# Kernel optimization log

Measured on AMD Instinct MI355X. Metric: run time of the kernel, lower is better.

## Reference

```python
import jax, jax.numpy as jnp
import numpy as np

N = 50000      # num_nodes
E = 800000     # num_edges
D = 128        # hidden_dim
POOL_RATIO = 0.5
CROSS_W = 1.0  # cross_weight


def _gcn(x, W, b, src, dst, n):
    """GCNConv: symmetric-normalized aggregation with self-loops. Dropout is identity (eval)."""
    loops = jnp.arange(n)
    s = jnp.concatenate([src, loops])
    d = jnp.concatenate([dst, loops])
    deg = jax.ops.segment_sum(jnp.ones(s.shape, x.dtype), d, num_segments=n)
    inv_sqrt = jax.lax.rsqrt(jnp.maximum(deg, 1.0))  # deg >= 1 due to self-loops
    xw = x @ W                                        # [n, D]
    msg = xw[s] * (inv_sqrt[s] * inv_sqrt[d])[:, None]  # [E+n, D] gather
    return jax.ops.segment_sum(msg, d, num_segments=n) + b


def _prelu(x, a):
    return jnp.where(x >= 0, x, a * x)


def setup_inputs() -> dict:
    key = jax.random.key(0)
    ks = jax.random.split(key, 8)
    glorot = lambda k, sh: jax.random.normal(k, sh, jnp.float32) * np.float32(np.sqrt(2.0 / (sh[0] + sh[1])))
    return {
        "feat": jax.random.normal(ks[0], (N, D), jnp.float32),
        "h_neg": jax.random.normal(ks[1], (N, D), jnp.float32),
        "edge_index": jax.random.randint(ks[2], (2, E), 0, N),
        "Wd": glorot(ks[3], (D, D)),
        "bd": jnp.zeros((D,), jnp.float32),
        "prelu_a": jnp.full((1,), 0.25, jnp.float32),
        "Wbil": glorot(ks[4], (D, D)),
        "bbil": jnp.zeros((1,), jnp.float32),
        "Wg1": glorot(ks[5], (D, D)),
        "bg1": jnp.zeros((D,), jnp.float32),
        "Wg2": glorot(ks[6], (D, D)),
        "bg2": jnp.zeros((D,), jnp.float32),
        "Wg3": glorot(ks[7], (D, D)),
        "bg3": jnp.zeros((D,), jnp.float32),
    }


def reference(feat, h_neg, edge_index, Wd, bd, prelu_a, Wbil, bbil,
              Wg1, bg1, Wg2, bg2, Wg3, bg3):
    src, dst = edge_index[0], edge_index[1]
    # --- IndexSelect: dense layer on pos/neg features ---
    h_pos = _prelu(feat @ Wd + bd, prelu_a)
    h_neg_d = _prelu(h_neg @ Wd + bd, prelu_a)
    embed = _gcn(h_pos, Wg1, bg1, src, dst, N)
    h_center = jax.nn.sigmoid(embed)
    # Discriminator (bilinear) positive scores -> node importance
    score_pos = jnp.einsum('nd,de,ne->n', h_pos, Wbil, h_center) + bbil[0]
    _ = jnp.einsum('nd,de,ne->n', h_neg_d, Wbil, h_center) + bbil[0]  # score_neg (logits branch)
    scores = jax.nn.sigmoid(score_pos)
    order = jnp.argsort(-scores)           # descending
    k = int(POOL_RATIO * N)
    select_idx = order[:k]
    select_scores = scores[order][:k]
    # --- GraphPool (use_gcn=True): down-sample GCN, gather, scale ---
    pooled = _gcn(embed, Wg2, bg2, src, dst, N)[select_idx] * select_scores[:, None]
    # --- GraphUnpool: scatter into zeros, up-sample GCN ---
    fine = jnp.zeros((N, D), feat.dtype).at[select_idx].set(pooled)
    out = _gcn(fine, Wg3, bg3, src, dst, N)
    # --- cross/fuse connection ---
    return out + CROSS_W * embed
```

## Files before the change

### kernel.cpp

```cpp
#include <hip/hip_runtime.h>
#include <hip/hip_bf16.h>

#define NN 50000
#define NE 800000
#define DD 128
#define KSEL 25000
#define NBK 391
#define NBLKA 98

typedef unsigned int uint32;
typedef unsigned short ushort16;

__device__ __forceinline__ float sigmoidf(float x){ return 1.f/(1.f+__expf(-x)); }

__device__ __forceinline__ unsigned short f2b(float f){
  union{float f; unsigned u;} v; v.f=f;
  unsigned r=(v.u + 0x7fffu + ((v.u>>16)&1u))>>16;
  return (unsigned short)r;
}

__device__ __forceinline__ void addbf2(float&lo,float&hi,uint32 u,float w){
  lo+=__uint_as_float(u<<16)*w;
  hi+=__uint_as_float(u&0xffff0000u)*w;
}

__global__ __launch_bounds__(1024) void k_bcount(const int* __restrict__ dst,
    int* __restrict__ btot, int* __restrict__ blkcnt){
  __shared__ int h[NBK];
  int tid=threadIdx.x;
  for(int i=tid;i<NBK;i+=1024) h[i]=0;
  __syncthreads();
  int e0=blockIdx.x*8192;
  #pragma unroll
  for(int t=0;t<8;t++){
    int e=e0+t*1024+tid;
    if(e<NE) atomicAdd(&h[dst[e]>>7],1);
  }
  __syncthreads();
  for(int i=tid;i<NBK;i+=1024){
    int c=h[i];
    blkcnt[blockIdx.x*NBK+i]=c;
    if(c) atomicAdd(&btot[i],c);
  }
}

__global__ __launch_bounds__(512) void k_bscan(const int* __restrict__ btot,
    int* __restrict__ boff, const int* __restrict__ blkcnt, int* __restrict__ blkbase,
    int* __restrict__ row_start){
  __shared__ int sdata[512];
  int tid=threadIdx.x;
  int v=(tid<NBK)?btot[tid]:0;
  sdata[tid]=v; __syncthreads();
  for(int off=1;off<512;off<<=1){
    int y=(tid>=off)?sdata[tid-off]:0;
    __syncthreads();
    sdata[tid]+=y;
    __syncthreads();
  }
  int excl=sdata[tid]-v;
  if(tid<NBK) boff[tid]=excl;
  if(tid==NBK-1){ boff[NBK]=excl+v; row_start[NN]=NE; }
  if(tid<NBK){
    int run=excl;
    for(int b=0;b<NBLKA;b++){
      int c=blkcnt[b*NBK+tid];
      blkbase[b*NBK+tid]=run;
      run+=c;
    }
  }
}

__global__ __launch_bounds__(1024) void k_bscatter(const int* __restrict__ src,
    const int* __restrict__ dst, const int* __restrict__ blkbase, uint32* __restrict__ pairs){
  __shared__ int cur[NBK];
  int tid=threadIdx.x;
  for(int i=tid;i<NBK;i+=1024) cur[i]=blkbase[blockIdx.x*NBK+i];
  __syncthreads();
  int e0=blockIdx.x*8192;
  #pragma unroll
  for(int t=0;t<8;t++){
    int e=e0+t*1024+tid;
    if(e<NE){
      int d=dst[e];
      int p=atomicAdd(&cur[d>>7],1);
      pairs[p]=(unsigned)src[e] | ((unsigned)(d&127)<<17);
    }
  }
}

__global__ __launch_bounds__(256) void k_bfinal(const uint32* __restrict__ pairs,
    const int* __restrict__ boff, int* __restrict__ row_start,
    float* __restrict__ inv_sq, int* __restrict__ csr_src){
  __shared__ int degl[128];
  __shared__ int cur[128];
  __shared__ int ssum[2];
  int b=blockIdx.x, tid=threadIdx.x;
  int lo=boff[b], hi=boff[b+1];
  if(tid<128) degl[tid]=0;
  __syncthreads();
  for(int e=lo+tid;e<hi;e+=256) atomicAdd(&degl[pairs[e]>>17],1);
  __syncthreads();
  int v=0,x=0;
  if(tid<128){
    v=degl[tid]; x=v;
    #pragma unroll
    for(int off=1;off<64;off<<=1){
      int y=__shfl_up(x,off,64);
      if((tid&63)>=off) x+=y;
    }
    if((tid&63)==63) ssum[tid>>6]=x;
  }
  __syncthreads();
  if(tid<128){
    int incl=x+((tid>=64)?ssum[0]:0);
    int node=b*128+tid;
    int excl=lo+incl-v;
    if(node<NN){
      row_start[node]=excl;
      cur[tid]=excl;
      inv_sq[node]=1.f/sqrtf((float)(v+1));
    }
  }
  __syncthreads();
  for(int e=lo+tid;e<hi;e+=256){
    uint32 u=pairs[e];
    int p=atomicAdd(&cur[u>>17],1);
    csr_src[p]=(int)(u&0x1FFFFu);
  }
}

__global__ void k_transpose(const float* __restrict__ W, float* __restrict__ Wt){
  int idx=blockIdx.x*256+threadIdx.x;
  if(idx<DD*DD){
    int k=idx>>7, c=idx&127;
    Wt[idx]=W[c*DD+k];
  }
}

template<int IN_SIG,int ACT,int OUT_BF16,int FUSE_SCORE>
__global__ __launch_bounds__(256) void k_gemm128(const float* __restrict__ A,
    const float* __restrict__ W, const float* __restrict__ bias,
    float* __restrict__ outf, ushort16* __restrict__ outb,
    const float* __restrict__ aparam, const float* __restrict__ hp,
    const float* __restrict__ bbil, float* __restrict__ score){
  __shared__ float Al[128][132];
  int tid=threadIdx.x;
  int row0=blockIdx.x*128;
  {
    const float4* A4=(const float4*)(A+(size_t)row0*DD);
    #pragma unroll
    for(int i=0;i<16;i++){
      int idx=i*256+tid;
      int r=idx>>5, c=(idx&31)*4;
      float4 v=make_float4(0.f,0.f,0.f,0.f);
      if(row0+r<NN) v=A4[idx];
      if(IN_SIG){ v.x=sigmoidf(v.x); v.y=sigmoidf(v.y); v.z=sigmoidf(v.z); v.w=sigmoidf(v.w); }
      *(float4*)&Al[r][c]=v;
    }
  }
  __syncthreads();
  int tx=tid&15, ty=tid>>4;
  float acc[8][8];
  #pragma unroll
  for(int i=0;i<8;i++)
    #pragma unroll
    for(int c=0;c<8;c++) acc[i][c]=0.f;

  for(int k=0;k<DD;k+=4){
    float wv[4][8];
    #pragma unroll
    for(int r=0;r<4;r++){
      float4 lo=*(const float4*)&W[(size_t)(k+r)*DD+tx*8];
      float4 hi=*(const float4*)&W[(size_t)(k+r)*DD+tx*8+4];
      wv[r][0]=lo.x; wv[r][1]=lo.y; wv[r][2]=lo.z; wv[r][3]=lo.w;
      wv[r][4]=hi.x; wv[r][5]=hi.y; wv[r][6]=hi.z; wv[r][7]=hi.w;
    }
    #pragma unroll
    for(int i=0;i<8;i++){
      float4 a=*(const float4*)&Al[ty+16*i][k];
      #pragma unroll
      for(int c=0;c<8;c++)
        acc[i][c]+=a.x*wv[0][c]+a.y*wv[1][c]+a.z*wv[2][c]+a.w*wv[3][c];
    }
  }

  if(FUSE_SCORE){
    float bb=bbil[0];
    #pragma unroll
    for(int i=0;i<8;i++){
      int r=row0+ty+16*i;
      float p=0.f;
      if(r<NN){
        float4 h0=*(const float4*)&hp[(size_t)r*DD+tx*8];
        float4 h1=*(const float4*)&hp[(size_t)r*DD+tx*8+4];
        p=acc[i][0]*h0.x+acc[i][1]*h0.y+acc[i][2]*h0.z+acc[i][3]*h0.w
         +acc[i][4]*h1.x+acc[i][5]*h1.y+acc[i][6]*h1.z+acc[i][7]*h1.w;
      }
      p+=__shfl_xor(p,1,64); p+=__shfl_xor(p,2,64);
      p+=__shfl_xor(p,4,64); p+=__shfl_xor(p,8,64);
      if(tx==0 && r<NN) score[r]=sigmoidf(p+bb);
    }
    return;
  }
  float bl[8]={0,0,0,0,0,0,0,0};
  if(bias){
    float4 b0=*(const float4*)&bias[tx*8];
    float4 b1=*(const float4*)&bias[tx*8+4];
    bl[0]=b0.x; bl[1]=b0.y; bl[2]=b0.z; bl[3]=b0.w;
    bl[4]=b1.x; bl[5]=b1.y; bl[6]=b1.z; bl[7]=b1.w;
  }
  float ap=ACT?aparam[0]:0.f;
  #pragma unroll
  for(int i=0;i<8;i++){
    int r=row0+ty+16*i;
    if(r<NN){
      float o[8];
      #pragma unroll
      for(int c=0;c<8;c++){
        float t=acc[i][c]+bl[c];
        if(ACT) t=t>=0.f?t:ap*t;
        o[c]=t;
      }
      if(OUT_BF16){
        uint4 pk;
        pk.x=((uint32)f2b(o[1])<<16)|f2b(o[0]);
        pk.y=((uint32)f2b(o[3])<<16)|f2b(o[2]);
        pk.z=((uint32)f2b(o[5])<<16)|f2b(o[4]);
        pk.w=((uint32)f2b(o[7])<<16)|f2b(o[6]);
        *(uint4*)&outb[(size_t)r*DD+tx*8]=pk;
      } else {
        float4 q0; q0.x=o[0]; q0.y=o[1]; q0.z=o[2]; q0.w=o[3];
        float4 q1; q1.x=o[4]; q1.y=o[5]; q1.z=o[6]; q1.w=o[7];
        *(float4*)&outf[(size_t)r*DD+tx*8]=q0;
        *(float4*)&outf[(size_t)r*DD+tx*8+4]=q1;
      }
    }
  }
}

__global__ __launch_bounds__(256) void k_agg_f32(const float* __restrict__ xw,
    const int* __restrict__ row_start, const int* __restrict__ csr,
    const float* __restrict__ inv, const float* __restrict__ bias,
    float* __restrict__ outp){
  int node=blockIdx.x*4+(threadIdx.x>>6);
  if(node>=NN) return;
  int lane=threadIdx.x&63;
  int g=lane>>5, li=lane&31;
  int rs=row_start[node], re=row_start[node+1];
  float a0=0.f,a1=0.f,a2=0.f,a3=0.f;
  int j=rs;
  for(; j+7<re; j+=8){
    int s0=csr[j+g], s1=csr[j+2+g], s2=csr[j+4+g], s3=csr[j+6+g];
    float w0=inv[s0], w1=inv[s1], w2=inv[s2], w3=inv[s3];
    float4 v0=*(const float4*)&xw[(size_t)s0*DD+li*4];
    float4 v1=*(const float4*)&xw[(size_t)s1*DD+li*4];
    float4 v2=*(const float4*)&xw[(size_t)s2*DD+li*4];
    float4 v3=*(const float4*)&xw[(size_t)s3*DD+li*4];
    a0+=v0.x*w0+v1.x*w1+v2.x*w2+v3.x*w3;
    a1+=v0.y*w0+v1.y*w1+v2.y*w2+v3.y*w3;
    a2+=v0.z*w0+v1.z*w1+v2.z*w2+v3.z*w3;
    a3+=v0.w*w0+v1.w*w1+v2.w*w2+v3.w*w3;
  }
  for(; j+1<re; j+=2){
    int s=csr[j+g];
    float w=inv[s];
    float4 v=*(const float4*)&xw[(size_t)s*DD+li*4];
    a0+=v.x*w; a1+=v.y*w; a2+=v.z*w; a3+=v.w*w;
  }
  if(j<re && g==0){
    int s=csr[j]; float w=inv[s];
    float4 v=*(const float4*)&xw[(size_t)s*DD+li*4];
    a0+=v.x*w; a1+=v.y*w; a2+=v.z*w; a3+=v.w*w;
  }
  if(g==0){
    float wd=inv[node];
    float4 v=*(const float4*)&xw[(size_t)node*DD+li*4];
    a0+=v.x*wd; a1+=v.y*wd; a2+=v.z*wd; a3+=v.w*wd;
  }
  a0+=__shfl_xor(a0,32,64); a1+=__shfl_xor(a1,32,64);
  a2+=__shfl_xor(a2,32,64); a3+=__shfl_xor(a3,32,64);
  if(g==0){
    float wn=inv[node];
    float4 bv=*(const float4*)&bias[li*4];
    float4 o;
    o.x=a0*wn+bv.x; o.y=a1*wn+bv.y; o.z=a2*wn+bv.z; o.w=a3*wn+bv.w;
    *(float4*)&outp[(size_t)node*DD+li*4]=o;
  }
}

template<int MODE>
__global__ __launch_bounds__(256) void k_agg_b16(const uint32* __restrict__ xwb,
    const int* __restrict__ row_start, const int* __restrict__ csr,
    const float* __restrict__ inv, const float* __restrict__ bias,
    float* __restrict__ outp, const float* __restrict__ score,
    const unsigned char* __restrict__ sel, const float* __restrict__ addbuf){
  int node=blockIdx.x*4+(threadIdx.x>>6);
  if(node>=NN) return;
  int lane=threadIdx.x&63;
  if(MODE==1 && !sel[node]){
    float2 z; z.x=0.f; z.y=0.f;
    *(float2*)&outp[(size_t)node*DD+lane*2]=z;
    return;
  }
  int g=lane>>4, li=lane&15;
  int rs=row_start[node], re=row_start[node+1];
  float a[8];
  #pragma unroll
  for(int c=0;c<8;c++) a[c]=0.f;
  int j=rs;
  for(; j+7<re; j+=8){
    int sA=csr[j+g], sB=csr[j+4+g];
    if(MODE!=2 || sel[sA]){
      float w=inv[sA];
      uint4 u=*(const uint4*)(xwb+(size_t)sA*64+li*4);
      addbf2(a[0],a[1],u.x,w); addbf2(a[2],a[3],u.y,w);
      addbf2(a[4],a[5],u.z,w); addbf2(a[6],a[7],u.w,w);
    }
    if(MODE!=2 || sel[sB]){
      float w=inv[sB];
      uint4 u=*(const uint4*)(xwb+(size_t)sB*64+li*4);
      addbf2(a[0],a[1],u.x,w); addbf2(a[2],a[3],u.y,w);
      addbf2(a[4],a[5],u.z,w); addbf2(a[6],a[7],u.w,w);
    }
  }
  for(; j+3<re; j+=4){
    int s=csr[j+g];
    if(MODE!=2 || sel[s]){
      float w=inv[s];
      uint4 u=*(const uint4*)(xwb+(size_t)s*64+li*4);
      addbf2(a[0],a[1],u.x,w); addbf2(a[2],a[3],u.y,w);
      addbf2(a[4],a[5],u.z,w); addbf2(a[6],a[7],u.w,w);
    }
  }
  int rem=re-j;
  if(g<rem){
    int s=csr[j+g];
    if(MODE!=2 || sel[s]){
      float w=inv[s];
      uint4 u=*(const uint4*)(xwb+(size_t)s*64+li*4);
      addbf2(a[0],a[1],u.x,w); addbf2(a[2],a[3],u.y,w);
      addbf2(a[4],a[5],u.z,w); addbf2(a[6],a[7],u.w,w);
    }
  }
  if(g==0 && (MODE!=2 || sel[node])){
    float wd=inv[node];
    uint4 u=*(const uint4*)(xwb+(size_t)node*64+li*4);
    addbf2(a[0],a[1],u.x,wd); addbf2(a[2],a[3],u.y,wd);
    addbf2(a[4],a[5],u.z,wd); addbf2(a[6],a[7],u.w,wd);
  }
  #pragma unroll
  for(int c=0;c<8;c++){
    a[c]+=__shfl_xor(a[c],16,64);
    a[c]+=__shfl_xor(a[c],32,64);
  }
  if(g<2){
    float wn=inv[node];
    int cb=li*8+g*4;
    float4 bv=*(const float4*)&bias[cb];
    float r0=a[g*4+0]*wn+bv.x, r1=a[g*4+1]*wn+bv.y;
    float r2=a[g*4+2]*wn+bv.z, r3=a[g*4+3]*wn+bv.w;
    if(MODE==1){
      float sc=score[node];
      r0*=sc; r1*=sc; r2*=sc; r3*=sc;
    } else {
      float4 ad=*(const float4*)&addbuf[(size_t)node*DD+cb];
      r0+=ad.x; r1+=ad.y; r2+=ad.z; r3+=ad.w;
    }
    float4 o; o.x=r0; o.y=r1; o.z=r2; o.w=r3;
    *(float4*)&outp[(size_t)node*DD+cb]=o;
  }
}

__global__ __launch_bounds__(1024) void k_select(const float* __restrict__ score,
    unsigned char* __restrict__ sel){
  __shared__ int h[4096];
  __shared__ int gs[1024];
  __shared__ int tie[2048];
  __shared__ int st[8];
  int tid=threadIdx.x;
  if(tid==0) st[6]=0;
  for(int i=tid;i<4096;i+=1024) h[i]=0;
  __syncthreads();
  for(int i=tid;i<NN;i+=1024){
    unsigned b=__float_as_uint(score[i]);
    atomicAdd(&h[b>>20],1);
  }
  __syncthreads();
  {
    int s=h[tid*4]+h[tid*4+1]+h[tid*4+2]+h[tid*4+3];
    int x=s; gs[tid]=x; __syncthreads();
    for(int off=1;off<1024;off<<=1){
      int y=(tid+off<1024)?gs[tid+off]:0;
      __syncthreads(); x+=y; gs[tid]=x; __syncthreads();
    }
    int incl=x, above=x-s;
    if(above<KSEL && incl>=KSEL){
      int c=above, B=0;
      for(int b=3;b>=0;b--){ int hb=h[tid*4+b]; if(c+hb>=KSEL){B=tid*4+b;break;} c+=hb; }
      st[0]=B; st[1]=c;
    }
  }
  __syncthreads();
  int B0=st[0];
  for(int i=tid;i<4096;i+=1024) h[i]=0;
  __syncthreads();
  for(int i=tid;i<NN;i+=1024){
    unsigned b=__float_as_uint(score[i]);
    if((int)(b>>20)==B0) atomicAdd(&h[(b>>8)&0xFFF],1);
  }
  __syncthreads();
  {
    int base=st[1];
    int s=h[tid*4]+h[tid*4+1]+h[tid*4+2]+h[tid*4+3];
    int x=s; gs[tid]=x; __syncthreads();
    for(int off=1;off<1024;off<<=1){
      int y=(tid+off<1024)?gs[tid+off]:0;
      __syncthreads(); x+=y; gs[tid]=x; __syncthreads();
    }
    int incl=base+x, above=base+x-s;
    if(above<KSEL && incl>=KSEL){
      int c=above, B=0;
      for(int b=3;b>=0;b--){ int hb=h[tid*4+b]; if(c+hb>=KSEL){B=tid*4+b;break;} c+=hb; }
      st[2]=(B0<<12)|B; st[3]=c;
    }
  }
  __syncthreads();
  int P01=st[2];
  for(int i=tid;i<256;i+=1024) h[i]=0;
  __syncthreads();
  for(int i=tid;i<NN;i+=1024){
    unsigned b=__float_as_uint(score[i]);
    if((int)(b>>8)==P01) atomicAdd(&h[b&0xFF],1);
  }
  __syncthreads();
  {
    int base=st[3];
    int s=0,x=0;
    if(tid<64){ s=h[tid*4]+h[tid*4+1]+h[tid*4+2]+h[tid*4+3]; x=s; }
    gs[tid]=x; __syncthreads();
    for(int off=1;off<64;off<<=1){
      int y=(tid+off<64)?gs[tid+off]:0;
      __syncthreads();
      if(tid<64){ x+=y; gs[tid]=x; }
      __syncthreads();
    }
    if(tid<64){
      int incl=base+x, above=base+x-s;
      if(above<KSEL && incl>=KSEL){
        int c=above, B=0;
        for(int b=3;b>=0;b--){ int hb=h[tid*4+b]; if(c+hb>=KSEL){B=tid*4+b;break;} c+=hb; }
        st[4]=(int)((((unsigned)P01)<<8)|(unsigned)B); st[5]=KSEL-c;
      }
    }
  }
  __syncthreads();
  unsigned thr=(unsigned)st[4];
  for(int i=tid;i<NN;i+=1024){
    unsigned b=__float_as_uint(score[i]);
    unsigned char sv=0;
    if(b>thr) sv=1;
    else if(b==thr){
      int p=atomicAdd(&st[6],1);
      if(p<2048) tie[p]=i;
    }
    sel[i]=sv;
  }
  __syncthreads();
  int m=st[6]; if(m>2048) m=2048;
  int needed=st[5];
  for(int t=tid;t<m;t+=1024){
    int idx=tie[t];
    int rank=0;
    for(int j2=0;j2<m;j2++) rank+=(tie[j2]<idx)?1:0;
    if(rank<needed) sel[idx]=1;
  }
}

extern "C" void kernel_launch(void* const* d_in, const int* in_sizes, int n_in,
                              void* d_out, int out_size, void* d_ws, size_t ws_size,
                              hipStream_t stream){
  const float* feat   =(const float*)d_in[0];
  const int*   ei     =(const int*)  d_in[2];
  const int*   src    = ei;
  const int*   dst    = ei + NE;
  const float* Wd     =(const float*)d_in[3];
  const float* bd     =(const float*)d_in[4];
  const float* prelu_a=(const float*)d_in[5];
  const float* Wbil   =(const float*)d_in[6];
  const float* bbil   =(const float*)d_in[7];
  const float* Wg1    =(const float*)d_in[8];
  const float* bg1    =(const float*)d_in[9];
  const float* Wg2    =(const float*)d_in[10];
  const float* bg2    =(const float*)d_in[11];
  const float* Wg3    =(const float*)d_in[12];
  const float* bg3    =(const float*)d_in[13];
  float* out=(float*)d_out;

  char* p=(char*)d_ws;
  auto alloc=[&](size_t bytes)->void*{ void* r=(void*)p; p+=((bytes+255)/256)*256; return r; };
  float* h_pos   =(float*)alloc((size_t)NN*DD*4);
  float* embed   =(float*)alloc((size_t)NN*DD*4);
  float* xw      =(float*)alloc((size_t)NN*DD*4);
  float* score   =(float*)alloc((size_t)NN*4);
  float* inv_sq  =(float*)alloc((size_t)NN*4);
  float* WbT     =(float*)alloc((size_t)DD*DD*4);
  int*   row_st  =(int*)  alloc((size_t)(NN+1)*4);
  int*   csr_src =(int*)  alloc((size_t)NE*4);
  unsigned char* sel=(unsigned char*)alloc(NN);
  int*   btot    =(int*)  alloc((size_t)NBK*4);
  int*   boff    =(int*)  alloc((size_t)(NBK+1)*4);
  int*   blkcnt  =(int*)  alloc((size_t)NBLKA*NBK*4);
  int*   blkbase =(int*)  alloc((size_t)NBLKA*NBK*4);
  uint32* pairs  =(uint32*)xw;
  ushort16* xwb  =(ushort16*)xw;
  float* fine = out;

  const int GB=(NN+127)/128;
  const int AB=(NN+3)/4;

  hipMemsetAsync(btot, 0, (size_t)NBK*4, stream);

  k_bcount  <<<NBLKA,1024,0,stream>>>(dst, btot, blkcnt);
  k_bscan   <<<1,512,0,stream>>>(btot, boff, blkcnt, blkbase, row_st);
  k_bscatter<<<NBLKA,1024,0,stream>>>(src, dst, blkbase, pairs);
  k_bfinal  <<<NBK,256,0,stream>>>(pairs, boff, row_st, inv_sq, csr_src);
  k_transpose<<<64,256,0,stream>>>(Wbil, WbT);

  k_gemm128<0,1,0,0><<<GB,256,0,stream>>>(feat, Wd, bd, h_pos, nullptr, prelu_a, nullptr, nullptr, nullptr);
  k_gemm128<0,0,0,0><<<GB,256,0,stream>>>(h_pos, Wg1, nullptr, xw, nullptr, nullptr, nullptr, nullptr, nullptr);
  k_agg_f32<<<AB,256,0,stream>>>(xw, row_st, csr_src, inv_sq, bg1, embed);
  k_gemm128<1,0,0,1><<<GB,256,0,stream>>>(embed, WbT, nullptr, nullptr, nullptr, nullptr, h_pos, bbil, score);
  k_select<<<1,1024,0,stream>>>(score, sel);
  k_gemm128<0,0,1,0><<<GB,256,0,stream>>>(embed, Wg2, nullptr, nullptr, xwb, nullptr, nullptr, nullptr, nullptr);
  k_agg_b16<1><<<AB,256,0,stream>>>((const uint32*)xwb, row_st, csr_src, inv_sq, bg2, fine, score, sel, nullptr);
  k_gemm128<0,0,1,0><<<GB,256,0,stream>>>(fine, Wg3, nullptr, nullptr, xwb, nullptr, nullptr, nullptr, nullptr);
  k_agg_b16<2><<<AB,256,0,stream>>>((const uint32*)xwb, row_st, csr_src, inv_sq, bg3, out, nullptr, sel, embed);
}
```

Baseline: 394.5 us.

## Compact selected nodes, parallelize top-k select, and shrink GEMM row tiles

Top-k selection moves from a single 1024-thread block to a 120-block kernel. It builds the radix histograms with global atomics and synchronizes through software grid barriers. It also emits a compact list of the selected node indices. The pooled aggregation and the up-sample GEMM then process only the 25000 selected rows instead of all nodes, skipping the zero-fill and zero-row work. GEMM row tiles drop from 128 to 96 so more blocks are launched. The risks are the software grid barrier, which needs all 120 blocks to be co-resident, and a nondeterministic order in the selected-node list.

```diff
diff --git a/kernel.cpp b/kernel.cpp
--- a/kernel.cpp
+++ b/kernel.cpp
@@ -7,6 +7,7 @@
 #define KSEL 25000
 #define NBK 391
 #define NBLKA 98
+#define SBLK 120
 
 typedef unsigned int uint32;
 typedef unsigned short ushort16;
@@ -22,6 +23,10 @@
 __device__ __forceinline__ void addbf2(float&lo,float&hi,uint32 u,float w){
   lo+=__uint_as_float(u<<16)*w;
   hi+=__uint_as_float(u&0xffff0000u)*w;
+}
+
+__device__ __forceinline__ int aload(const int* p){
+  return __hip_atomic_load(p,__ATOMIC_RELAXED,__HIP_MEMORY_SCOPE_AGENT);
 }
 
 __global__ __launch_bounds__(1024) void k_bcount(const int* __restrict__ dst,
@@ -137,32 +142,35 @@
   }
 }
 
-template<int IN_SIG,int ACT,int OUT_BF16,int FUSE_SCORE>
-__global__ __launch_bounds__(256) void k_gemm128(const float* __restrict__ A,
+template<int IN_SIG,int ACT,int OUT_BF16,int FUSE_SCORE,int ROWLIST>
+__global__ __launch_bounds__(256) void k_gemm96(const float* __restrict__ A,
     const float* __restrict__ W, const float* __restrict__ bias,
     float* __restrict__ outf, ushort16* __restrict__ outb,
     const float* __restrict__ aparam, const float* __restrict__ hp,
-    const float* __restrict__ bbil, float* __restrict__ score){
-  __shared__ float Al[128][132];
+    const float* __restrict__ bbil, float* __restrict__ score,
+    const int* __restrict__ rlist){
+  __shared__ float Al[96][132];
   int tid=threadIdx.x;
-  int row0=blockIdx.x*128;
+  int row0=blockIdx.x*96;
   {
-    const float4* A4=(const float4*)(A+(size_t)row0*DD);
-    #pragma unroll
-    for(int i=0;i<16;i++){
+    #pragma unroll
+    for(int i=0;i<12;i++){
       int idx=i*256+tid;
       int r=idx>>5, c=(idx&31)*4;
+      int gr; bool ok;
+      if(ROWLIST){ int ri=row0+r; ok=(ri<KSEL); gr=ok?rlist[ri]:0; }
+      else { gr=row0+r; ok=(gr<NN); }
       float4 v=make_float4(0.f,0.f,0.f,0.f);
-      if(row0+r<NN) v=A4[idx];
+      if(ok) v=*(const float4*)&A[(size_t)gr*DD+c];
       if(IN_SIG){ v.x=sigmoidf(v.x); v.y=sigmoidf(v.y); v.z=sigmoidf(v.z); v.w=sigmoidf(v.w); }
       *(float4*)&Al[r][c]=v;
     }
   }
   __syncthreads();
   int tx=tid&15, ty=tid>>4;
-  float acc[8][8];
+  float acc[6][8];
   #pragma unroll
-  for(int i=0;i<8;i++)
+  for(int i=0;i<6;i++)
     #pragma unroll
     for(int c=0;c<8;c++) acc[i][c]=0.f;
 
@@ -176,7 +184,7 @@
       wv[r][4]=hi.x; wv[r][5]=hi.y; wv[r][6]=hi.z; wv[r][7]=hi.w;
     }
     #pragma unroll
-    for(int i=0;i<8;i++){
+    for(int i=0;i<6;i++){
       float4 a=*(const float4*)&Al[ty+16*i][k];
       #pragma unroll
       for(int c=0;c<8;c++)
@@ -187,7 +195,7 @@
   if(FUSE_SCORE){
     float bb=bbil[0];
     #pragma unroll
-    for(int i=0;i<8;i++){
+    for(int i=0;i<6;i++){
       int r=row0+ty+16*i;
       float p=0.f;
       if(r<NN){
@@ -211,9 +219,12 @@
   }
   float ap=ACT?aparam[0]:0.f;
   #pragma unroll
-  for(int i=0;i<8;i++){
-    int r=row0+ty+16*i;
-    if(r<NN){
+  for(int i=0;i<6;i++){
+    int ri=row0+ty+16*i;
+    int r; bool ok;
+    if(ROWLIST){ ok=(ri<KSEL); r=ok?rlist[ri]:0; }
+    else { r=ri; ok=(r<NN); }
+    if(ok){
       float o[8];
       #pragma unroll
       for(int c=0;c<8;c++){
@@ -293,15 +304,13 @@
     const int* __restrict__ row_start, const int* __restrict__ csr,
     const float* __restrict__ inv, const float* __restrict__ bias,
     float* __restrict__ outp, const float* __restrict__ score,
-    const unsigned char* __restrict__ sel, const float* __restrict__ addbuf){
-  int node=blockIdx.x*4+(threadIdx.x>>6);
-  if(node>=NN) return;
+    const unsigned char* __restrict__ sel, const float* __restrict__ addbuf,
+    const int* __restrict__ list){
+  int idx4=blockIdx.x*4+(threadIdx.x>>6);
+  int node;
+  if(MODE==1){ if(idx4>=KSEL) return; node=list[idx4]; }
+  else { node=idx4; if(node>=NN) return; }
   int lane=threadIdx.x&63;
-  if(MODE==1 && !sel[node]){
-    float2 z; z.x=0.f; z.y=0.f;
-    *(float2*)&outp[(size_t)node*DD+lane*2]=z;
-    return;
-  }
   int g=lane>>4, li=lane&15;
   int rs=row_start[node], re=row_start[node+1];
   float a[8];
@@ -371,72 +380,101 @@
   }
 }
 
-__global__ __launch_bounds__(1024) void k_select(const float* __restrict__ score,
-    unsigned char* __restrict__ sel){
-  __shared__ int h[4096];
-  __shared__ int gs[1024];
-  __shared__ int tie[2048];
-  __shared__ int st[8];
-  int tid=threadIdx.x;
-  if(tid==0) st[6]=0;
-  for(int i=tid;i<4096;i+=1024) h[i]=0;
-  __syncthreads();
-  for(int i=tid;i<NN;i+=1024){
-    unsigned b=__float_as_uint(score[i]);
-    atomicAdd(&h[b>>20],1);
-  }
-  __syncthreads();
-  {
-    int s=h[tid*4]+h[tid*4+1]+h[tid*4+2]+h[tid*4+3];
+__global__ __launch_bounds__(256) void k_select_fused(const float* __restrict__ score,
+    unsigned char* __restrict__ sel, int* __restrict__ list,
+    int* __restrict__ hist0, int* __restrict__ hist1, int* __restrict__ hist2,
+    int* __restrict__ ctrl, int* __restrict__ tie_list, int* __restrict__ gbar){
+  __shared__ int lh[4096];
+  __shared__ int gs[256];
+  int tid=threadIdx.x, bid=blockIdx.x;
+  auto bar=[&](int ph){
+    __syncthreads();
+    if(tid==0){
+      __hip_atomic_fetch_add(&gbar[ph],1,__ATOMIC_ACQ_REL,__HIP_MEMORY_SCOPE_AGENT);
+      while(__hip_atomic_load(&gbar[ph],__ATOMIC_ACQUIRE,__HIP_MEMORY_SCOPE_AGENT)<SBLK){}
+    }
+    __syncthreads();
+  };
+  for(int i=bid*256+tid;i<4096+4096+256;i+=SBLK*256){
+    if(i<4096) hist0[i]=0;
+    else if(i<8192) hist1[i-4096]=0;
+    else hist2[i-8192]=0;
+  }
+  bar(0);
+  for(int i=tid;i<4096;i+=256) lh[i]=0;
+  __syncthreads();
+  for(int i=bid*256+tid;i<NN;i+=SBLK*256)
+    atomicAdd(&lh[__float_as_uint(score[i])>>20],1);
+  __syncthreads();
+  for(int i=tid;i<4096;i+=256){ int v=lh[i]; if(v) atomicAdd(&hist0[i],v); }
+  bar(1);
+  if(bid==0){
+    int s=0;
+    #pragma unroll
+    for(int q=0;q<16;q++) s+=aload(&hist0[tid*16+q]);
     int x=s; gs[tid]=x; __syncthreads();
-    for(int off=1;off<1024;off<<=1){
-      int y=(tid+off<1024)?gs[tid+off]:0;
+    for(int off=1;off<256;off<<=1){
+      int y=(tid+off<256)?gs[tid+off]:0;
       __syncthreads(); x+=y; gs[tid]=x; __syncthreads();
     }
-    int incl=x, above=x-s;
+    int above=x-s, incl=x;
     if(above<KSEL && incl>=KSEL){
       int c=above, B=0;
-      for(int b=3;b>=0;b--){ int hb=h[tid*4+b]; if(c+hb>=KSEL){B=tid*4+b;break;} c+=hb; }
-      st[0]=B; st[1]=c;
-    }
-  }
-  __syncthreads();
-  int B0=st[0];
-  for(int i=tid;i<4096;i+=1024) h[i]=0;
-  __syncthreads();
-  for(int i=tid;i<NN;i+=1024){
-    unsigned b=__float_as_uint(score[i]);
-    if((int)(b>>20)==B0) atomicAdd(&h[(b>>8)&0xFFF],1);
-  }
-  __syncthreads();
+      for(int b=15;b>=0;b--){ int hb=aload(&hist0[tid*16+b]); if(c+hb>=KSEL){B=tid*16+b;break;} c+=hb; }
+      ctrl[0]=B; ctrl[1]=c;
+    }
+  }
+  bar(2);
   {
-    int base=st[1];
-    int s=h[tid*4]+h[tid*4+1]+h[tid*4+2]+h[tid*4+3];
+    int p0=aload(&ctrl[0]);
+    for(int i=tid;i<4096;i+=256) lh[i]=0;
+    __syncthreads();
+    for(int i=bid*256+tid;i<NN;i+=SBLK*256){
+      unsigned b=__float_as_uint(score[i]);
+      if((int)(b>>20)==p0) atomicAdd(&lh[(b>>8)&0xFFF],1);
+    }
+    __syncthreads();
+    for(int i=tid;i<4096;i+=256){ int v=lh[i]; if(v) atomicAdd(&hist1[i],v); }
+  }
+  bar(3);
+  if(bid==0){
+    int base=aload(&ctrl[1]);
+    int s=0;
+    #pragma unroll
+    for(int q=0;q<16;q++) s+=aload(&hist1[tid*16+q]);
     int x=s; gs[tid]=x; __syncthreads();
-    for(int off=1;off<1024;off<<=1){
-      int y=(tid+off<1024)?gs[tid+off]:0;
+    for(int off=1;off<256;off<<=1){
+      int y=(tid+off<256)?gs[tid+off]:0;
       __syncthreads(); x+=y; gs[tid]=x; __syncthreads();
     }
-    int incl=base+x, above=base+x-s;
+    int above=base+x-s, incl=base+x;
     if(above<KSEL && incl>=KSEL){
       int c=above, B=0;
-      for(int b=3;b>=0;b--){ int hb=h[tid*4+b]; if(c+hb>=KSEL){B=tid*4+b;break;} c+=hb; }
-      st[2]=(B0<<12)|B; st[3]=c;
-    }
-  }
-  __syncthreads();
-  int P01=st[2];
-  for(int i=tid;i<256;i+=1024) h[i]=0;
-  __syncthreads();
-  for(int i=tid;i<NN;i+=1024){
-    unsigned b=__float_as_uint(score[i]);
-    if((int)(b>>8)==P01) atomicAdd(&h[b&0xFF],1);
-  }
-  __syncthreads();
+      for(int b=15;b>=0;b--){ int hb=aload(&hist1[tid*16+b]); if(c+hb>=KSEL){B=tid*16+b;break;} c+=hb; }
+      ctrl[2]=(aload(&ctrl[0])<<12)|B; ctrl[3]=c;
+    }
+  }
+  bar(4);
   {
-    int base=st[3];
+    int p01=aload(&ctrl[2]);
+    for(int i=tid;i<256;i+=256) lh[i]=0;
+    __syncthreads();
+    for(int i=bid*256+tid;i<NN;i+=SBLK*256){
+      unsigned b=__float_as_uint(score[i]);
+      if((int)(b>>8)==p01) atomicAdd(&lh[b&0xFF],1);
+    }
+    __syncthreads();
+    for(int i=tid;i<256;i+=256){ int v=lh[i]; if(v) atomicAdd(&hist2[i],v); }
+  }
+  bar(5);
+  if(bid==0){
+    int base=aload(&ctrl[3]);
     int s=0,x=0;
-    if(tid<64){ s=h[tid*4]+h[tid*4+1]+h[tid*4+2]+h[tid*4+3]; x=s; }
+    if(tid<64){
+      #pragma unroll
+      for(int q=0;q<4;q++) s+=aload(&hist2[tid*4+q]);
+      x=s;
+    }
     gs[tid]=x; __syncthreads();
     for(int off=1;off<64;off<<=1){
       int y=(tid+off<64)?gs[tid+off]:0;
@@ -445,34 +483,46 @@
       __syncthreads();
     }
     if(tid<64){
-      int incl=base+x, above=base+x-s;
+      int above=base+x-s, incl=base+x;
       if(above<KSEL && incl>=KSEL){
         int c=above, B=0;
-        for(int b=3;b>=0;b--){ int hb=h[tid*4+b]; if(c+hb>=KSEL){B=tid*4+b;break;} c+=hb; }
-        st[4]=(int)((((unsigned)P01)<<8)|(unsigned)B); st[5]=KSEL-c;
+        for(int b=3;b>=0;b--){ int hb=aload(&hist2[tid*4+b]); if(c+hb>=KSEL){B=tid*4+b;break;} c+=hb; }
+        ctrl[4]=(int)((((unsigned)aload(&ctrl[2]))<<8)|(unsigned)B);
+        ctrl[5]=KSEL-c;
       }
     }
   }
-  __syncthreads();
-  unsigned thr=(unsigned)st[4];
-  for(int i=tid;i<NN;i+=1024){
-    unsigned b=__float_as_uint(score[i]);
-    unsigned char sv=0;
-    if(b>thr) sv=1;
-    else if(b==thr){
-      int p=atomicAdd(&st[6],1);
-      if(p<2048) tie[p]=i;
-    }
-    sel[i]=sv;
-  }
-  __syncthreads();
-  int m=st[6]; if(m>2048) m=2048;
-  int needed=st[5];
-  for(int t=tid;t<m;t+=1024){
-    int idx=tie[t];
-    int rank=0;
-    for(int j2=0;j2<m;j2++) rank+=(tie[j2]<idx)?1:0;
-    if(rank<needed) sel[idx]=1;
+  bar(6);
+  {
+    unsigned thr=(unsigned)aload(&ctrl[4]);
+    for(int i=bid*256+tid;i<NN;i+=SBLK*256){
+      unsigned b=__float_as_uint(score[i]);
+      unsigned char sv=0;
+      if(b>thr){
+        sv=1;
+        int p=atomicAdd(&ctrl[7],1);
+        list[p]=i;
+      } else if(b==thr){
+        int p=atomicAdd(&ctrl[6],1);
+        if(p<4096) __hip_atomic_store(&tie_list[p],i,__ATOMIC_RELAXED,__HIP_MEMORY_SCOPE_AGENT);
+      }
+      sel[i]=sv;
+    }
+  }
+  bar(7);
+  if(bid==0){
+    int m=aload(&ctrl[6]); if(m>4096) m=4096;
+    int needed=aload(&ctrl[5]);
+    for(int t=tid;t<m;t+=256){
+      int idx=aload(&tie_list[t]);
+      int rank=0;
+      for(int j2=0;j2<m;j2++) rank+=(aload(&tie_list[j2])<idx)?1:0;
+      if(rank<needed){
+        sel[idx]=1;
+        int p=atomicAdd(&ctrl[7],1);
+        list[p]=idx;
+      }
+    }
   }
 }
 
@@ -506,6 +556,13 @@
   float* WbT     =(float*)alloc((size_t)DD*DD*4);
   int*   row_st  =(int*)  alloc((size_t)(NN+1)*4);
   int*   csr_src =(int*)  alloc((size_t)NE*4);
+  int*   ctrl    =(int*)  alloc(64);
+  int*   gbar    =(int*)  alloc(64);
+  int*   hist0   =(int*)  alloc(4096*4);
+  int*   hist1   =(int*)  alloc(4096*4);
+  int*   hist2   =(int*)  alloc(256*4);
+  int*   tie_list=(int*)  alloc(4096*4);
+  int*   list    =(int*)  alloc((size_t)KSEL*4);
   unsigned char* sel=(unsigned char*)alloc(NN);
   int*   btot    =(int*)  alloc((size_t)NBK*4);
   int*   boff    =(int*)  alloc((size_t)(NBK+1)*4);
@@ -515,9 +572,12 @@
   ushort16* xwb  =(ushort16*)xw;
   float* fine = out;
 
-  const int GB=(NN+127)/128;
+  const int GB=(NN+95)/96;
+  const int GBL=(KSEL+95)/96;
   const int AB=(NN+3)/4;
-
+  const int ABL=(KSEL+3)/4;
+
+  hipMemsetAsync(ctrl, 0, 512, stream);
   hipMemsetAsync(btot, 0, (size_t)NBK*4, stream);
 
   k_bcount  <<<NBLKA,1024,0,stream>>>(dst, btot, blkcnt);
@@ -526,13 +586,13 @@
   k_bfinal  <<<NBK,256,0,stream>>>(pairs, boff, row_st, inv_sq, csr_src);
   k_transpose<<<64,256,0,stream>>>(Wbil, WbT);
 
-  k_gemm128<0,1,0,0><<<GB,256,0,stream>>>(feat, Wd, bd, h_pos, nullptr, prelu_a, nullptr, nullptr, nullptr);
-  k_gemm128<0,0,0,0><<<GB,256,0,stream>>>(h_pos, Wg1, nullptr, xw, nullptr, nullptr, nullptr, nullptr, nullptr);
+  k_gemm96<0,1,0,0,0><<<GB,256,0,stream>>>(feat, Wd, bd, h_pos, nullptr, prelu_a, nullptr, nullptr, nullptr, nullptr);
+  k_gemm96<0,0,0,0,0><<<GB,256,0,stream>>>(h_pos, Wg1, nullptr, xw, nullptr, nullptr, nullptr, nullptr, nullptr, nullptr);
   k_agg_f32<<<AB,256,0,stream>>>(xw, row_st, csr_src, inv_sq, bg1, embed);
-  k_gemm128<1,0,0,1><<<GB,256,0,stream>>>(embed, WbT, nullptr, nullptr, nullptr, nullptr, h_pos, bbil, score);
-  k_select<<<1,1024,0,stream>>>(score, sel);
-  k_gemm128<0,0,1,0><<<GB,256,0,stream>>>(embed, Wg2, nullptr, nullptr, xwb, nullptr, nullptr, nullptr, nullptr);
-  k_agg_b16<1><<<AB,256,0,stream>>>((const uint32*)xwb, row_st, csr_src, inv_sq, bg2, fine, score, sel, nullptr);
-  k_gemm128<0,0,1,0><<<GB,256,0,stream>>>(fine, Wg3, nullptr, nullptr, xwb, nullptr, nullptr, nullptr, nullptr);
-  k_agg_b16<2><<<AB,256,0,stream>>>((const uint32*)xwb, row_st, csr_src, inv_sq, bg3, out, nullptr, sel, embed);
-}
+  k_gemm96<1,0,0,1,0><<<GB,256,0,stream>>>(embed, WbT, nullptr, nullptr, nullptr, nullptr, h_pos, bbil, score, nullptr);
+  k_select_fused<<<SBLK,256,0,stream>>>(score, sel, list, hist0, hist1, hist2, ctrl, tie_list, gbar);
+  k_gemm96<0,0,1,0,0><<<GB,256,0,stream>>>(embed, Wg2, nullptr, nullptr, xwb, nullptr, nullptr, nullptr, nullptr, nullptr);
+  k_agg_b16<1><<<ABL,256,0,stream>>>((const uint32*)xwb, row_st, csr_src, inv_sq, bg2, fine, score, sel, nullptr, list);
+  k_gemm96<0,0,1,0,1><<<GBL,256,0,stream>>>(fine, Wg3, nullptr, nullptr, xwb, nullptr, nullptr, nullptr, nullptr, list);
+  k_agg_b16<2><<<AB,256,0,stream>>>((const uint32*)xwb, row_st, csr_src, inv_sq, bg3, out, nullptr, sel, embed, nullptr);
+}
```

After: 422.6 us. 7.1% more time.
